# Optimization experiments

Hardware: AMD Instinct MI355X
Metric: run time of the kernel (lower is better)

## Reference

```python
import jax, jax.numpy as jnp
import numpy as np

B, S, E, L = 8, 2048, 512, 128


def setup_inputs() -> dict:
    key = jax.random.key(0)
    k1, k2 = jax.random.split(key)
    embeddings = jax.random.normal(k1, (B, S, E), dtype=jnp.float32)
    means = jax.random.normal(k2, (L, E), dtype=jnp.float32)
    var = jnp.ones((E,), dtype=jnp.float32)  # default init: requires_grad=False, ones
    return {"embeddings": embeddings, "means": means, "var": var}


def reference(embeddings, means, var):
    # Diagonal-Gaussian log-density per (token, label):
    #   log_density - 0.5 * sum_e (means[l,e] - emb[b,s,e])^2 / var[e]
    # Rewritten as GEMM + per-row/per-label norms (avoids [B,S,L,E] intermediate).
    n_embed = embeddings.shape[-1]
    factor = -n_embed / 2.0 * (np.log(2.0) + np.log(np.pi))
    # After init_params: log_density = factor - 0.5 * sum(log var); var=ones -> factor.
    log_density = factor - 0.5 * jnp.sum(jnp.log(var))
    inv_var = 1.0 / var  # [E]
    e2 = jnp.einsum('bse,e->bs', embeddings * embeddings, inv_var)      # [B,S]
    m2 = jnp.einsum('le,e->l', means * means, inv_var)                  # [L]
    cross = jnp.einsum('bse,le->bsl', embeddings, means * inv_var)      # [B,S,L]
    sq_mahalanobis = e2[..., None] + m2[None, None, :] - 2.0 * cross    # [B,S,L]
    return log_density - 0.5 * sq_mahalanobis
```

## Files before the change

kernel.cpp:

```cpp
#include <hip/hip_runtime.h>
#include <math.h>

#define EDIM 512
#define LDIM 128
#define MTOT 16384
#define TM 32
#define BK 64
#define LSTR 72

typedef __attribute__((ext_vector_type(8))) short s8v;
typedef __attribute__((ext_vector_type(4))) float f4v;

__device__ __forceinline__ unsigned short f2bf(float x) {
    union { float f; unsigned u; } c; c.f = x;
    return (unsigned short)((c.u + 0x7fffu + ((c.u >> 16) & 1u)) >> 16);
}

__device__ __forceinline__ void ld_lds16(const void* g, void* l) {
    __builtin_amdgcn_global_load_lds(
        (const __attribute__((address_space(1))) unsigned int*)g,
        (__attribute__((address_space(3))) unsigned int*)l, 16, 0, 0);
}

__global__ __launch_bounds__(64) void gs_prep(
    const float* __restrict__ means, const float* __restrict__ var,
    unsigned short* __restrict__ Bmat, float* __restrict__ m2,
    float* __restrict__ ivbuf, float* __restrict__ coef)
{
    const int l = blockIdx.x;
    const int t = threadIdx.x;
    const int e0 = t * 8;

    float mv[8], iv[8];
    const float* mrow = means + l * EDIM + e0;
#pragma unroll
    for (int i = 0; i < 8; ++i) { mv[i] = mrow[i]; iv[i] = 1.0f / var[e0 + i]; }

    float part = 0.0f;
    s8v pr;
#pragma unroll
    for (int i = 0; i < 8; ++i) {
        float p = mv[i] * iv[i];
        pr[i] = (short)f2bf(p);
        part += mv[i] * p;
    }
    *(s8v*)(Bmat + l * EDIM + e0) = pr;

#pragma unroll
    for (int off = 32; off > 0; off >>= 1) part += __shfl_down(part, off, 64);
    if (t == 0) m2[l] = part;

    if (l == 0) {
#pragma unroll
        for (int i = 0; i < 8; ++i) ivbuf[e0 + i] = iv[i];
        float ld = 0.0f;
#pragma unroll
        for (int i = 0; i < 8; ++i) ld += logf(var[e0 + i]);
#pragma unroll
        for (int off = 32; off > 0; off >>= 1) ld += __shfl_down(ld, off, 64);
        if (t == 0) {
            const float factor = -(float)EDIM * 0.5f * 1.8378770664093453f;
            *coef = factor - 0.5f * ld;
        }
    }
}

__global__ __launch_bounds__(256) void gs_main(
    const float* __restrict__ emb, const unsigned short* __restrict__ Bmat,
    const float* __restrict__ m2, const float* __restrict__ ivbuf,
    const float* __restrict__ coef, float* __restrict__ out)
{
    __shared__ __align__(16) unsigned short Alds[2][TM][LSTR];
    __shared__ __align__(16) unsigned short Blds[2][16 * 64 * 8];
    __shared__ float e2part[256];
    __shared__ float e2s[TM];

    const int t    = threadIdx.x;
    const int lane = t & 63;
    const int w    = t >> 6;
    const int q    = lane >> 4;
    const int fr   = lane & 15;
    const int m0   = blockIdx.x * TM;

    const int arow = t >> 3;
    const int kseg = (t & 7) * 8;

    const int r0w = (w >> 1) * 16;
    const int c0w1 = (w & 1) * 4;

    const float* ap  = emb   + (size_t)(m0 + arow) * EDIM + kseg;
    const float* ivp = ivbuf + kseg;

    f4v acc[4];
#pragma unroll
    for (int i = 0; i < 4; ++i) acc[i] = (f4v)0.0f;
    float e2acc = 0.0f;

    f4v ar0[2], ar1[2], vr0[2], vr1[2];
    ar0[0] = *(const f4v*)(ap);          ar1[0] = *(const f4v*)(ap + 4);
    ar0[1] = *(const f4v*)(ap + BK);     ar1[1] = *(const f4v*)(ap + BK + 4);
    vr0[0] = *(const f4v*)(ivp);         vr1[0] = *(const f4v*)(ivp + 4);
    vr0[1] = *(const f4v*)(ivp + BK);    vr1[1] = *(const f4v*)(ivp + BK + 4);

#define STAGE_B(kc, buf)                                                        \
    {                                                                           \
        _Pragma("unroll")                                                       \
        for (int j = 0; j < 4; ++j) {                                           \
            const int F   = w * 4 + j;                                          \
            const int col = (F & 7) * 16 + fr;                                  \
            const int kk  = (kc) * BK + (F >> 3) * 32 + q * 8;                  \
            ld_lds16(Bmat + col * EDIM + kk, (void*)&Blds[buf][F * 512]);       \
        }                                                                       \
    }

    STAGE_B(0, 0)

#pragma unroll
    for (int kc = 0; kc < EDIM / BK; ++kc) {
        const int b = kc & 1;

        f4v xa = ar0[b], xb = ar1[b], va = vr0[b], vb = vr1[b];
        s8v a8;
#pragma unroll
        for (int i = 0; i < 4; ++i) {
            a8[i] = (short)f2bf(xa[i]);
            e2acc += xa[i] * xa[i] * va[i];
        }
#pragma unroll
        for (int i = 0; i < 4; ++i) {
            a8[4 + i] = (short)f2bf(xb[i]);
            e2acc += xb[i] * xb[i] * vb[i];
        }
        *(s8v*)&Alds[b][arow][kseg] = a8;

        __syncthreads();

        if (kc + 1 < EDIM / BK) STAGE_B(kc + 1, b ^ 1)
        if (kc + 2 < EDIM / BK) {
            const int k2 = (kc + 2) * BK;
            ar0[b] = *(const f4v*)(ap + k2);  ar1[b] = *(const f4v*)(ap + k2 + 4);
            vr0[b] = *(const f4v*)(ivp + k2); vr1[b] = *(const f4v*)(ivp + k2 + 4);
        }

#pragma unroll
        for (int ks_i = 0; ks_i < 2; ++ks_i) {
            s8v af = *(const s8v*)&Alds[b][r0w + fr][ks_i * 32 + q * 8];
#pragma unroll
            for (int ct = 0; ct < 4; ++ct) {
                const int F = ks_i * 8 + c0w1 + ct;
                s8v bfv = *(const s8v*)&Blds[b][F * 512 + lane * 8];
                acc[ct] = __builtin_amdgcn_mfma_f32_16x16x32_bf16(af, bfv, acc[ct], 0, 0, 0);
            }
        }
    }

    e2part[t] = e2acc;
    __syncthreads();
    if (t < TM) {
        float s = 0.0f;
#pragma unroll
        for (int j = 0; j < 8; ++j) s += e2part[t * 8 + j];
        e2s[t] = s;
    }
    __syncthreads();

    const float cf = *coef;
#pragma unroll
    for (int ct = 0; ct < 4; ++ct) {
        const int n = (c0w1 + ct) * 16 + fr;
        const float cm = cf - 0.5f * m2[n];
#pragma unroll
        for (int r = 0; r < 4; ++r) {
            const int row = r0w + q * 4 + r;
            out[(size_t)(m0 + row) * LDIM + n] = acc[ct][r] + cm - 0.5f * e2s[row];
        }
    }
#undef STAGE_B
}

extern "C" void kernel_launch(void* const* d_in, const int* in_sizes, int n_in,
                              void* d_out, int out_size, void* d_ws, size_t ws_size,
                              hipStream_t stream) {
    const float* emb   = (const float*)d_in[0];
    const float* means = (const float*)d_in[1];
    const float* var   = (const float*)d_in[2];
    float* out = (float*)d_out;

    char* ws = (char*)d_ws;
    unsigned short* Bmat = (unsigned short*)ws;
    float* m2    = (float*)(ws + 131072);
    float* ivbuf = (float*)(ws + 131584);
    float* coef  = (float*)(ws + 133632);

    gs_prep<<<LDIM, 64, 0, stream>>>(means, var, Bmat, m2, ivbuf, coef);
    gs_main<<<MTOT / TM, 256, 0, stream>>>(emb, Bmat, m2, ivbuf, coef, out);
}
```

Baseline: 90.14 us.

## Pre-swizzle B into MFMA fragment layout and halve row tile to 16

```diff
diff --git a/kernel.cpp b/kernel.cpp
--- a/kernel.cpp
+++ b/kernel.cpp
@@ -4,11 +4,13 @@
 #define EDIM 512
 #define LDIM 128
 #define MTOT 16384
-#define TM 32
+#define TM 16
 #define BK 64
+#define NCHUNK (EDIM / BK)
 #define LSTR 72
 
 typedef __attribute__((ext_vector_type(8))) short s8v;
+typedef __attribute__((ext_vector_type(4))) short s4v;
 typedef __attribute__((ext_vector_type(4))) float f4v;
 
 __device__ __forceinline__ unsigned short f2bf(float x) {
@@ -24,7 +26,7 @@
 
 __global__ __launch_bounds__(64) void gs_prep(
     const float* __restrict__ means, const float* __restrict__ var,
-    unsigned short* __restrict__ Bmat, float* __restrict__ m2,
+    unsigned short* __restrict__ Bfrag, float* __restrict__ m2,
     float* __restrict__ ivbuf, float* __restrict__ coef)
 {
     const int l = blockIdx.x;
@@ -44,7 +46,14 @@
         pr[i] = (short)f2bf(p);
         part += mv[i] * p;
     }
-    *(s8v*)(Bmat + l * EDIM + e0) = pr;
+    {
+        const int kc   = t >> 3;
+        const int ks_i = (t >> 2) & 1;
+        const int q    = t & 3;
+        const int F    = ks_i * 8 + (l >> 4);
+        const int ln   = q * 16 + (l & 15);
+        *(s8v*)(Bfrag + kc * 8192 + F * 512 + ln * 8) = pr;
+    }
 
 #pragma unroll
     for (int off = 32; off > 0; off >>= 1) part += __shfl_down(part, off, 64);
@@ -65,8 +74,8 @@
     }
 }
 
-__global__ __launch_bounds__(256) void gs_main(
-    const float* __restrict__ emb, const unsigned short* __restrict__ Bmat,
+__global__ __launch_bounds__(256, 4) void gs_main(
+    const float* __restrict__ emb, const unsigned short* __restrict__ Bfrag,
     const float* __restrict__ m2, const float* __restrict__ ivbuf,
     const float* __restrict__ coef, float* __restrict__ out)
 {
@@ -82,72 +91,58 @@
     const int fr   = lane & 15;
     const int m0   = blockIdx.x * TM;
 
-    const int arow = t >> 3;
-    const int kseg = (t & 7) * 8;
-
-    const int r0w = (w >> 1) * 16;
-    const int c0w1 = (w & 1) * 4;
+    const int arow = t >> 4;
+    const int kseg = (t & 15) * 4;
 
     const float* ap  = emb   + (size_t)(m0 + arow) * EDIM + kseg;
     const float* ivp = ivbuf + kseg;
 
-    f4v acc[4];
-#pragma unroll
-    for (int i = 0; i < 4; ++i) acc[i] = (f4v)0.0f;
+    f4v acc[2];
+    acc[0] = (f4v)0.0f; acc[1] = (f4v)0.0f;
     float e2acc = 0.0f;
 
-    f4v ar0[2], ar1[2], vr0[2], vr1[2];
-    ar0[0] = *(const f4v*)(ap);          ar1[0] = *(const f4v*)(ap + 4);
-    ar0[1] = *(const f4v*)(ap + BK);     ar1[1] = *(const f4v*)(ap + BK + 4);
-    vr0[0] = *(const f4v*)(ivp);         vr1[0] = *(const f4v*)(ivp + 4);
-    vr0[1] = *(const f4v*)(ivp + BK);    vr1[1] = *(const f4v*)(ivp + BK + 4);
+    f4v ar[2], vr[2];
+    ar[0] = *(const f4v*)(ap);        ar[1] = *(const f4v*)(ap + BK);
+    vr[0] = *(const f4v*)(ivp);       vr[1] = *(const f4v*)(ivp + BK);
 
-#define STAGE_B(kc, buf)                                                        \
-    {                                                                           \
-        _Pragma("unroll")                                                       \
-        for (int j = 0; j < 4; ++j) {                                           \
-            const int F   = w * 4 + j;                                          \
-            const int col = (F & 7) * 16 + fr;                                  \
-            const int kk  = (kc) * BK + (F >> 3) * 32 + q * 8;                  \
-            ld_lds16(Bmat + col * EDIM + kk, (void*)&Blds[buf][F * 512]);       \
-        }                                                                       \
+#define STAGE_B(kc, buf)                                                       \
+    {                                                                          \
+        const char* sb = (const char*)Bfrag + (kc) * 16384 + w * 4096;         \
+        char*       db = (char*)&Blds[buf][0] + w * 4096;                      \
+        _Pragma("unroll")                                                      \
+        for (int j = 0; j < 4; ++j)                                            \
+            ld_lds16(sb + j * 1024 + lane * 16, db + j * 1024);                \
     }
 
     STAGE_B(0, 0)
 
 #pragma unroll
-    for (int kc = 0; kc < EDIM / BK; ++kc) {
+    for (int kc = 0; kc < NCHUNK; ++kc) {
         const int b = kc & 1;
 
-        f4v xa = ar0[b], xb = ar1[b], va = vr0[b], vb = vr1[b];
-        s8v a8;
+        f4v xa = ar[b], va = vr[b];
+        s4v a4;
 #pragma unroll
         for (int i = 0; i < 4; ++i) {
-            a8[i] = (short)f2bf(xa[i]);
+            a4[i] = (short)f2bf(xa[i]);
             e2acc += xa[i] * xa[i] * va[i];
         }
-#pragma unroll
-        for (int i = 0; i < 4; ++i) {
-            a8[4 + i] = (short)f2bf(xb[i]);
-            e2acc += xb[i] * xb[i] * vb[i];
-        }
-        *(s8v*)&Alds[b][arow][kseg] = a8;
+        *(s4v*)&Alds[b][arow][kseg] = a4;
 
         __syncthreads();
 
-        if (kc + 1 < EDIM / BK) STAGE_B(kc + 1, b ^ 1)
-        if (kc + 2 < EDIM / BK) {
-            const int k2 = (kc + 2) * BK;
-            ar0[b] = *(const f4v*)(ap + k2);  ar1[b] = *(const f4v*)(ap + k2 + 4);
-            vr0[b] = *(const f4v*)(ivp + k2); vr1[b] = *(const f4v*)(ivp + k2 + 4);
+        if (kc + 1 < NCHUNK) STAGE_B(kc + 1, b ^ 1)
+        if (kc + 2 < NCHUNK) {
+            ar[b] = *(const f4v*)(ap + (kc + 2) * BK);
+            vr[b] = *(const f4v*)(ivp + (kc + 2) * BK);
         }
 
 #pragma unroll
         for (int ks_i = 0; ks_i < 2; ++ks_i) {
-            s8v af = *(const s8v*)&Alds[b][r0w + fr][ks_i * 32 + q * 8];
+            s8v af = *(const s8v*)&Alds[b][fr][ks_i * 32 + q * 8];
 #pragma unroll
-            for (int ct = 0; ct < 4; ++ct) {
-                const int F = ks_i * 8 + c0w1 + ct;
+            for (int ct = 0; ct < 2; ++ct) {
+                const int F = ks_i * 8 + w * 2 + ct;
                 s8v bfv = *(const s8v*)&Blds[b][F * 512 + lane * 8];
                 acc[ct] = __builtin_amdgcn_mfma_f32_16x16x32_bf16(af, bfv, acc[ct], 0, 0, 0);
             }
@@ -159,19 +154,19 @@
     if (t < TM) {
         float s = 0.0f;
 #pragma unroll
-        for (int j = 0; j < 8; ++j) s += e2part[t * 8 + j];
+        for (int j = 0; j < 16; ++j) s += e2part[t * 16 + j];
         e2s[t] = s;
     }
     __syncthreads();
 
     const float cf = *coef;
 #pragma unroll
-    for (int ct = 0; ct < 4; ++ct) {
-        const int n = (c0w1 + ct) * 16 + fr;
+    for (int ct = 0; ct < 2; ++ct) {
+        const int n = (w * 2 + ct) * 16 + fr;
         const float cm = cf - 0.5f * m2[n];
 #pragma unroll
         for (int r = 0; r < 4; ++r) {
-            const int row = r0w + q * 4 + r;
+            const int row = q * 4 + r;
             out[(size_t)(m0 + row) * LDIM + n] = acc[ct][r] + cm - 0.5f * e2s[row];
         }
     }
@@ -187,11 +182,11 @@
     float* out = (float*)d_out;
 
     char* ws = (char*)d_ws;
-    unsigned short* Bmat = (unsigned short*)ws;
+    unsigned short* Bfrag = (unsigned short*)ws;
     float* m2    = (float*)(ws + 131072);
     float* ivbuf = (float*)(ws + 131584);
     float* coef  = (float*)(ws + 133632);
 
-    gs_prep<<<LDIM, 64, 0, stream>>>(means, var, Bmat, m2, ivbuf, coef);
-    gs_main<<<MTOT / TM, 256, 0, stream>>>(emb, Bmat, m2, ivbuf, coef, out);
+    gs_prep<<<LDIM, 64, 0, stream>>>(means, var, Bfrag, m2, ivbuf, coef);
+    gs_main<<<MTOT / TM, 256, 0, stream>>>(emb, Bfrag, m2, ivbuf, coef, out);
 }
```

Result: faster. 86.03 us (-4.6%).
